# Kernel optimization log

Hardware: AMD Instinct MI355X
Metric: run time of the kernel (lower is better)

The kernel has to match this reference:

```python
import jax, jax.numpy as jnp
import numpy as np


def setup_inputs() -> dict:
    key = jax.random.key(0)
    k0, k1, k2, k3 = jax.random.split(key, 4)
    B, C = 32, 768
    t_h = t_w = 8
    s_h = s_w = 16
    N = t_h * t_w * 2 + s_h * s_w  # 384
    return {
        "x_v": jax.random.normal(k0, (B, N, C), jnp.float32),
        "x_i": jax.random.normal(k1, (B, N, C), jnp.float32),
        "qkv_w": jax.random.normal(k2, (3 * C, C), jnp.float32) * 0.02,
        "proj_w": jax.random.normal(k3, (C, C), jnp.float32) * 0.02,
        "proj_b": jnp.zeros((C,), jnp.float32),
        "t_h": t_h, "t_w": t_w, "s_h": s_h, "s_w": s_w,
        "num_heads": 12,
    }


def reference(x_v, x_i, qkv_w, proj_w, proj_b, t_h, t_w, s_h, s_w, num_heads):
    B, N, C = x_v.shape
    H = num_heads
    Dh = C // H
    scale = Dh ** (-0.5)
    mt = t_h * t_w * 2  # template tokens (two templates)

    # joint QKV projection over both modalities: [2B, N, C]
    x = jnp.concatenate([x_v, x_i], axis=0)
    qkv = (x @ qkv_w.T).reshape(2 * B, N, 3, H, Dh)
    qkv = jnp.transpose(qkv, (2, 0, 3, 1, 4))  # [3, 2B, H, N, Dh]
    q, k, v = qkv[0], qkv[1], qkv[2]
    qV, qI = q[:B], q[B:]
    kV, kI = k[:B], k[B:]
    vV, vI = v[:B], v[B:]

    q_mt_V, q_s_V = qV[:, :, :mt], qV[:, :, mt:]
    k_mt_V, k_s_V = kV[:, :, :mt], kV[:, :, mt:]
    v_mt_V, v_s_V = vV[:, :, :mt], vV[:, :, mt:]
    q_mt_I, q_s_I = qI[:, :, :mt], qI[:, :, mt:]
    k_mt_I, k_s_I = kI[:, :, :mt], kI[:, :, mt:]
    v_mt_I, v_s_I = vI[:, :, :mt], vI[:, :, mt:]

    # shared cross-modal template KV
    k_mt = jnp.concatenate([k_mt_V, k_mt_I], axis=2)
    v_mt = jnp.concatenate([v_mt_V, v_mt_I], axis=2)

    def attend(q_, k_, v_):
        a = jax.nn.softmax(jnp.einsum('bhqd,bhkd->bhqk', q_, k_) * scale, axis=-1)
        o = jnp.einsum('bhqk,bhkd->bhqd', a, v_)
        return o.transpose(0, 2, 1, 3).reshape(B, -1, C)

    # template branches: self-attention within own modality
    x_mt_V = attend(q_mt_V, k_mt_V, v_mt_V)
    x_mt_I = attend(q_mt_I, k_mt_I, v_mt_I)
    # search branches: attend to cross-modal templates + own search
    x_s_V = attend(q_s_V, jnp.concatenate([k_mt, k_s_V], axis=2),
                   jnp.concatenate([v_mt, v_s_V], axis=2))
    x_s_I = attend(q_s_I, jnp.concatenate([k_mt, k_s_I], axis=2),
                   jnp.concatenate([v_mt, v_s_I], axis=2))

    x_V = jnp.concatenate([x_mt_V, x_s_V], axis=1)
    x_I = jnp.concatenate([x_mt_I, x_s_I], axis=1)
    out = jnp.concatenate([x_V, x_I], axis=0) @ proj_w.T + proj_b
    return out[:B], out[B:]
```

## Files before the change

kernel.cpp:

```cpp
#include <hip/hip_runtime.h>

typedef __bf16 bf16;
typedef __bf16 bf16x4 __attribute__((ext_vector_type(4)));
typedef __bf16 bf16x8 __attribute__((ext_vector_type(8)));
typedef float f32x4 __attribute__((ext_vector_type(4)));

#define MFMA16(a,b,c) __builtin_amdgcn_mfma_f32_16x16x32_bf16((a),(b),(c),0,0,0)
#define SBAR() __builtin_amdgcn_s_barrier()
#define SCHED0() __builtin_amdgcn_sched_barrier(0)


__device__ inline void gload16(const bf16* g, bf16* l) {
  __builtin_amdgcn_global_load_lds(
      (const __attribute__((address_space(1))) void*)g,
      (__attribute__((address_space(3))) void*)l, 16, 0, 0);
}

__device__ inline void stage128(const bf16* __restrict__ gsrc,
                                bf16* lds_base, int tid, int wv) {
#pragma unroll
  for (int r = 0; r < 4; ++r) {
    int s = r * 256 + tid;
    int row = s >> 3;
    int chunk = (s & 7) ^ (row & 7);
    gload16(gsrc + (size_t)row * 768 + chunk * 8,
            lds_base + (size_t)(r * 256 + wv * 64) * 8);
  }
}

__device__ inline bf16x8 frag64(const bf16* buf, int row, int ks, int lg) {
  int slot = ((ks << 2) | lg) ^ (row & 7);
  return *(const bf16x8*)(buf + (size_t)row * 64 + slot * 8);
}

#define GEMM128_LOOP(APANEL, BPANEL, NTILES)                                    \
  do {                                                                          \
    stage128((APANEL), &As[0][0][0], tid, wv);                                  \
    stage128((BPANEL), &Bs[0][0][0], tid, wv);                                  \
    stage128((APANEL) + 64, &As[1][0][0], tid, wv);                             \
    stage128((BPANEL) + 64, &Bs[1][0][0], tid, wv);                             \
    asm volatile("s_waitcnt vmcnt(8)" ::: "memory"); SCHED0();                  \
    SBAR();                                                                     \
    int c = 0;                                                                  \
    for (int t = 0; t < (NTILES); ++t) {                                        \
      const bf16* Ab = &As[c][0][0];                                            \
      const bf16* Bb = &Bs[c][0][0];                                            \
      bf16x8 af[4][2], bfr[4][2];                                               \
      _Pragma("unroll")                                                         \
      for (int nf = 0; nf < 4; ++nf)                                            \
        _Pragma("unroll")                                                       \
        for (int ks = 0; ks < 2; ++ks)                                          \
          bfr[nf][ks] = frag64(Bb, wc + nf * 16 + lr, ks, lg);                  \
      _Pragma("unroll")                                                         \
      for (int mf = 0; mf < 4; ++mf)                                            \
        _Pragma("unroll")                                                       \
        for (int ks = 0; ks < 2; ++ks)                                          \
          af[mf][ks] = frag64(Ab, wr + mf * 16 + lr, ks, lg);                   \
      asm volatile("s_waitcnt lgkmcnt(0)" ::: "memory"); SCHED0();              \
      SBAR();              \
      if (t + 2 < (NTILES)) {                                                   \
        stage128((APANEL) + (t + 2) * 64, &As[c][0][0], tid, wv);               \
        stage128((BPANEL) + (t + 2) * 64, &Bs[c][0][0], tid, wv);               \
      }                                                                         \
      __builtin_amdgcn_s_setprio(1);                                            \
      _Pragma("unroll")                                                         \
      for (int mf = 0; mf < 4; ++mf)                                            \
        _Pragma("unroll")                                                       \
        for (int nf = 0; nf < 4; ++nf)                                          \
          _Pragma("unroll")                                                     \
          for (int ks = 0; ks < 2; ++ks)                                        \
            acc[mf][nf] = MFMA16(af[mf][ks], bfr[nf][ks], acc[mf][nf]);         \
      __builtin_amdgcn_s_setprio(0);                                            \
      if (t + 2 < (NTILES)) { asm volatile("s_waitcnt vmcnt(8)" ::: "memory"); }\
      else                  { asm volatile("s_waitcnt vmcnt(0)" ::: "memory"); }\
      SCHED0();                                                                 \
      SBAR();                       \
      c ^= 1;                                                                   \
    }                                                                           \
  } while (0)

__global__ __launch_bounds__(256) void convert1_kernel(
    const float* __restrict__ xv, const float* __restrict__ xi,
    const float* __restrict__ w, bf16* __restrict__ dst)
{
  const size_t NV = 9437184;
  const size_t NX = 18874368;
  const size_t NT = 20643840;
  for (size_t i = (size_t)blockIdx.x * 256 + threadIdx.x; i * 8 < NT;
       i += (size_t)gridDim.x * 256) {
    size_t e = i * 8;
    const float* src;
    if (e < NV)      src = xv + e;
    else if (e < NX) src = xi + (e - NV);
    else             src = w + (e - NX);
    f32x4 a = *(const f32x4*)src;
    f32x4 b = *(const f32x4*)(src + 4);
    bf16x8 r;
    r[0] = (bf16)a[0]; r[1] = (bf16)a[1]; r[2] = (bf16)a[2]; r[3] = (bf16)a[3];
    r[4] = (bf16)b[0]; r[5] = (bf16)b[1]; r[6] = (bf16)b[2]; r[7] = (bf16)b[3];
    *(bf16x8*)(dst + e) = r;
  }
}

__global__ __launch_bounds__(256) void convert2_kernel(
    const float* __restrict__ w, bf16* __restrict__ dst)
{
  size_t i = (size_t)blockIdx.x * 256 + threadIdx.x;
  size_t e = i * 8;
  if (e >= 589824) return;
  f32x4 a = *(const f32x4*)(w + e);
  f32x4 b = *(const f32x4*)(w + e + 4);
  bf16x8 r;
  r[0] = (bf16)a[0]; r[1] = (bf16)a[1]; r[2] = (bf16)a[2]; r[3] = (bf16)a[3];
  r[4] = (bf16)b[0]; r[5] = (bf16)b[1]; r[6] = (bf16)b[2]; r[7] = (bf16)b[3];
  *(bf16x8*)(dst + e) = r;
}

__global__ __launch_bounds__(256, 2) void qkv_kernel(
    const bf16* __restrict__ X, const bf16* __restrict__ W,
    bf16* __restrict__ Qo, bf16* __restrict__ Ko, bf16* __restrict__ VTo)
{
  __shared__ bf16 As[2][128][64];
  __shared__ bf16 Bs[2][128][64];
  int bid = blockIdx.x;
  int swz = (bid & 7) * 432 + (bid >> 3);
  const int nt = swz % 18, mt = swz / 18;
  const int m0 = mt * 128, n0 = nt * 128;
  const int tid = threadIdx.x;
  const int lane = tid & 63;
  const int wv = tid >> 6;
  const int wr = (wv >> 1) * 64, wc = (wv & 1) * 64;
  const int lr = lane & 15, lg = lane >> 4;

  const bf16* Xp = X + (size_t)m0 * 768;
  const bf16* Wp = W + (size_t)n0 * 768;

  f32x4 acc[4][4] = {};

  GEMM128_LOOP(Xp, Wp, 12);

#pragma unroll
  for (int mf = 0; mf < 4; ++mf)
#pragma unroll
    for (int nf = 0; nf < 4; ++nf) {
      int m = m0 + wr + mf * 16 + lg * 4;
      int n = n0 + wc + nf * 16 + lr;
      int bp = m / 384, tok = m - bp * 384;
      int comp = (n >= 1536) ? 2 : (n >= 768) ? 1 : 0;
      int rem = n - comp * 768;
      int hh = rem >> 6, d = rem & 63;
      if (comp == 2) {
        bf16x4 pk;
        pk[0] = (bf16)acc[mf][nf][0]; pk[1] = (bf16)acc[mf][nf][1];
        pk[2] = (bf16)acc[mf][nf][2]; pk[3] = (bf16)acc[mf][nf][3];
        *(bf16x4*)(VTo + (((size_t)bp * 12 + hh) * 64 + d) * 384 + tok) = pk;
      } else {
#pragma unroll
        for (int r = 0; r < 4; ++r) {
          size_t addr = (((size_t)bp * 12 + hh) * 384 + tok + r) * 64 + d;
          float val = acc[mf][nf][r];
          if (comp == 0) Qo[addr] = (bf16)(val * 0.125f);
          else           Ko[addr] = (bf16)val;
        }
      }
    }
}

__global__ __launch_bounds__(256) void attn_kernel(
    const bf16* __restrict__ Q, const bf16* __restrict__ K, const bf16* __restrict__ VT,
    bf16* __restrict__ ATT)
{
  __shared__ union {
    bf16 Qs[128][72];
    bf16 Ps[4][32][136];
  } u;
  __shared__ bf16 Ks[128][72];
  __shared__ bf16 VTs[64][136];

  const int bid = blockIdx.x;
  const int qb = bid % 3;
  const int h  = (bid / 3) % 12;
  const int bp = bid / 36;
  const int tid = threadIdx.x;
  const int lane = tid & 63;
  const int wv = tid >> 6;
  const int lr = lane & 15, lg = lane >> 4;

  const size_t bh384 = ((size_t)bp * 12 + h) * 384;
  const int q0 = qb * 128;

  for (int v = tid; v < 1024; v += 256) {
    int row = v >> 3, cg = (v & 7) * 8;
    *(bf16x8*)(&u.Qs[row][cg]) = *(const bf16x8*)(Q + (bh384 + q0 + row) * 64 + cg);
  }
  __syncthreads();

  bf16x8 qf[2][2];
#pragma unroll
  for (int mf = 0; mf < 2; ++mf)
#pragma unroll
    for (int ks = 0; ks < 2; ++ks)
      qf[mf][ks] = *(const bf16x8*)(&u.Qs[wv * 32 + mf * 16 + lr][ks * 32 + lg * 8]);

  f32x4 O[2][4] = {};
  float runmax[2] = {-1e30f, -1e30f}, runsum[2] = {0.f, 0.f};

  const int nchunks = (qb == 0) ? 1 : 4;
  for (int c = 0; c < nchunks; ++c) {
    int src_b, t0;
    if (qb == 0)      { src_b = bp;            t0 = 0; }
    else if (c == 0)  { src_b = bp & 31;       t0 = 0; }
    else if (c == 1)  { src_b = (bp & 31)+32;  t0 = 0; }
    else              { src_b = bp;            t0 = (c - 1) * 128; }
    const size_t kb  = (((size_t)src_b * 12 + h) * 384 + t0) * 64;
    const size_t vtb = ((size_t)src_b * 12 + h) * 64 * 384 + t0;

    __syncthreads();
    for (int v = tid; v < 1024; v += 256) {
      int row = v >> 3, cg = (v & 7) * 8;
      *(bf16x8*)(&Ks[row][cg]) = *(const bf16x8*)(K + kb + row * 64 + cg);
    }
    for (int v = tid; v < 1024; v += 256) {
      int d = v >> 4, p = (v & 15) * 8;
      *(bf16x8*)(&VTs[d][p]) = *(const bf16x8*)(VT + vtb + (size_t)d * 384 + p);
    }
    __syncthreads();

    f32x4 St[2][8] = {};
#pragma unroll
    for (int nf = 0; nf < 8; ++nf) {
#pragma unroll
      for (int ks = 0; ks < 2; ++ks) {
        bf16x8 kf = *(const bf16x8*)(&Ks[nf * 16 + lr][ks * 32 + lg * 8]);
        St[0][nf] = MFMA16(kf, qf[0][ks], St[0][nf]);
        St[1][nf] = MFMA16(kf, qf[1][ks], St[1][nf]);
      }
    }

    float rfq[2];
#pragma unroll
    for (int mf = 0; mf < 2; ++mf) {
      float mx = St[mf][0][0];
#pragma unroll
      for (int nf = 0; nf < 8; ++nf)
#pragma unroll
        for (int r = 0; r < 4; ++r) mx = fmaxf(mx, St[mf][nf][r]);
      mx = fmaxf(mx, __shfl_xor(mx, 16));
      mx = fmaxf(mx, __shfl_xor(mx, 32));
      float nm = fmaxf(runmax[mf], mx);
      rfq[mf] = __expf(runmax[mf] - nm);
      runmax[mf] = nm;
      float rs = 0.f;
#pragma unroll
      for (int nf = 0; nf < 8; ++nf)
#pragma unroll
        for (int r = 0; r < 4; ++r) {
          float p = __expf(St[mf][nf][r] - nm);
          St[mf][nf][r] = p;
          rs += p;
        }
      rs += __shfl_xor(rs, 16);
      rs += __shfl_xor(rs, 32);
      runsum[mf] = runsum[mf] * rfq[mf] + rs;
    }

#pragma unroll
    for (int mf = 0; mf < 2; ++mf)
#pragma unroll
      for (int nf = 0; nf < 8; ++nf) {
        bf16x4 pk;
        pk[0] = (bf16)St[mf][nf][0]; pk[1] = (bf16)St[mf][nf][1];
        pk[2] = (bf16)St[mf][nf][2]; pk[3] = (bf16)St[mf][nf][3];
        *(bf16x4*)(&u.Ps[wv][mf * 16 + lr][nf * 16 + lg * 4]) = pk;
      }

#pragma unroll
    for (int mf = 0; mf < 2; ++mf)
#pragma unroll
      for (int r = 0; r < 4; ++r) {
        float rr = __shfl(rfq[mf], (lg * 4 + r) + (lg << 4));
#pragma unroll
        for (int vn = 0; vn < 4; ++vn) O[mf][vn][r] *= rr;
      }

#pragma unroll
    for (int ks = 0; ks < 4; ++ks) {
      bf16x8 pf0 = *(const bf16x8*)(&u.Ps[wv][lr][ks * 32 + lg * 8]);
      bf16x8 pf1 = *(const bf16x8*)(&u.Ps[wv][16 + lr][ks * 32 + lg * 8]);
#pragma unroll
      for (int vn = 0; vn < 4; ++vn) {
        bf16x8 vf = *(const bf16x8*)(&VTs[vn * 16 + lr][ks * 32 + lg * 8]);
        O[0][vn] = MFMA16(pf0, vf, O[0][vn]);
        O[1][vn] = MFMA16(pf1, vf, O[1][vn]);
      }
    }
  }

#pragma unroll
  for (int mf = 0; mf < 2; ++mf) {
#pragma unroll
    for (int r = 0; r < 4; ++r) {
      float rs = __shfl(runsum[mf], (lg * 4 + r) + (lg << 4));
      float inv = 1.0f / rs;
#pragma unroll
      for (int vn = 0; vn < 4; ++vn) {
        int tok = q0 + wv * 32 + mf * 16 + lg * 4 + r;
        int d = vn * 16 + lr;
        ATT[((size_t)bp * 384 + tok) * 768 + h * 64 + d] = (bf16)(O[mf][vn][r] * inv);
      }
    }
  }
}

__global__ __launch_bounds__(256, 2) void proj_kernel(
    const bf16* __restrict__ A, const bf16* __restrict__ W,
    const float* __restrict__ bias, float* __restrict__ out)
{
  __shared__ bf16 As[2][128][64];
  __shared__ bf16 Bs[2][128][64];
  int bid = blockIdx.x;
  int swz = (bid & 7) * 144 + (bid >> 3);
  const int nt = swz % 6, mt = swz / 6;
  const int m0 = mt * 128, n0 = nt * 128;
  const int tid = threadIdx.x;
  const int lane = tid & 63;
  const int wv = tid >> 6;
  const int wr = (wv >> 1) * 64, wc = (wv & 1) * 64;
  const int lr = lane & 15, lg = lane >> 4;

  const bf16* Ap = A + (size_t)m0 * 768;
  const bf16* Wpp = W + (size_t)n0 * 768;

  f32x4 acc[4][4] = {};

  GEMM128_LOOP(Ap, Wpp, 12);

#pragma unroll
  for (int mf = 0; mf < 4; ++mf)
#pragma unroll
    for (int nf = 0; nf < 4; ++nf)
#pragma unroll
      for (int r = 0; r < 4; ++r) {
        int m = m0 + wr + mf * 16 + lg * 4 + r;
        int n = n0 + wc + nf * 16 + lr;
        out[(size_t)m * 768 + n] = acc[mf][nf][r] + bias[n];
      }
}

extern "C" void kernel_launch(void* const* d_in, const int* in_sizes, int n_in,
                              void* d_out, int out_size, void* d_ws, size_t ws_size,
                              hipStream_t stream) {
  (void)in_sizes; (void)n_in; (void)out_size; (void)ws_size;
  const float* xv     = (const float*)d_in[0];
  const float* xi     = (const float*)d_in[1];
  const float* qkv_w  = (const float*)d_in[2];
  const float* proj_w = (const float*)d_in[3];
  const float* proj_b = (const float*)d_in[4];
  float* out = (float*)d_out;

  bf16* Xb = (bf16*)d_out;
  bf16* Wq = Xb + (size_t)18874368;

  const size_t SZ = (size_t)64 * 12 * 384 * 64;
  bf16* Q   = (bf16*)d_ws;
  bf16* K   = Q + SZ;
  bf16* VT  = K + SZ;
  bf16* ATT = VT + SZ;
  bf16* Wp  = Q;

  convert1_kernel<<<2048, 256, 0, stream>>>(xv, xi, qkv_w, Xb);
  qkv_kernel<<<3456, 256, 0, stream>>>(Xb, Wq, Q, K, VT);
  attn_kernel<<<64 * 12 * 3, 256, 0, stream>>>(Q, K, VT, ATT);
  convert2_kernel<<<288, 256, 0, stream>>>(proj_w, Wp);
  proj_kernel<<<1152, 256, 0, stream>>>(ATT, Wp, proj_b, out);
}
```

Before: 270.3 us.

## Prefetch next K/V chunk into registers in attention; use nontemporal stores

The attention kernel now loads the next chunk's K and V^T tiles into registers while the current chunk's QK^T and softmax/PV math runs, then writes them to LDS at the top of the next iteration. This hides global load latency behind compute at the cost of 8 extra bf16x8 registers per thread. Separately, the convert, QKV, and projection kernels switch their global writes to nontemporal stores. The aim is to avoid polluting caches with data consumed later, but the Q/K/V outputs are reread soon by attention, so bypassing the cache could also hurt.

```diff
diff --git a/kernel.cpp b/kernel.cpp
--- a/kernel.cpp
+++ b/kernel.cpp
@@ -98,7 +98,7 @@
     bf16x8 r;
     r[0] = (bf16)a[0]; r[1] = (bf16)a[1]; r[2] = (bf16)a[2]; r[3] = (bf16)a[3];
     r[4] = (bf16)b[0]; r[5] = (bf16)b[1]; r[6] = (bf16)b[2]; r[7] = (bf16)b[3];
-    *(bf16x8*)(dst + e) = r;
+    __builtin_nontemporal_store(r, (bf16x8*)(dst + e));
   }
 }
 
@@ -113,7 +113,7 @@
   bf16x8 r;
   r[0] = (bf16)a[0]; r[1] = (bf16)a[1]; r[2] = (bf16)a[2]; r[3] = (bf16)a[3];
   r[4] = (bf16)b[0]; r[5] = (bf16)b[1]; r[6] = (bf16)b[2]; r[7] = (bf16)b[3];
-  *(bf16x8*)(dst + e) = r;
+  __builtin_nontemporal_store(r, (bf16x8*)(dst + e));
 }
 
 __global__ __launch_bounds__(256, 2) void qkv_kernel(
@@ -153,14 +153,17 @@
         bf16x4 pk;
         pk[0] = (bf16)acc[mf][nf][0]; pk[1] = (bf16)acc[mf][nf][1];
         pk[2] = (bf16)acc[mf][nf][2]; pk[3] = (bf16)acc[mf][nf][3];
-        *(bf16x4*)(VTo + (((size_t)bp * 12 + hh) * 64 + d) * 384 + tok) = pk;
+        __builtin_nontemporal_store(
+            pk, (bf16x4*)(VTo + (((size_t)bp * 12 + hh) * 64 + d) * 384 + tok));
       } else {
 #pragma unroll
         for (int r = 0; r < 4; ++r) {
           size_t addr = (((size_t)bp * 12 + hh) * 384 + tok + r) * 64 + d;
           float val = acc[mf][nf][r];
-          if (comp == 0) Qo[addr] = (bf16)(val * 0.125f);
-          else           Ko[addr] = (bf16)val;
+          if (comp == 0)
+            __builtin_nontemporal_store((bf16)(val * 0.125f), Qo + addr);
+          else
+            __builtin_nontemporal_store((bf16)val, Ko + addr);
         }
       }
     }
@@ -188,6 +191,17 @@
 
   const size_t bh384 = ((size_t)bp * 12 + h) * 384;
   const int q0 = qb * 128;
+  const int nchunks = (qb == 0) ? 1 : 4;
+
+  auto chunk_base = [&](int c, size_t& kb, size_t& vtb) {
+    int src_b, t0;
+    if (qb == 0)      { src_b = bp;             t0 = 0; }
+    else if (c == 0)  { src_b = bp & 31;        t0 = 0; }
+    else if (c == 1)  { src_b = (bp & 31) + 32; t0 = 0; }
+    else              { src_b = bp;             t0 = (c - 1) * 128; }
+    kb  = (((size_t)src_b * 12 + h) * 384 + t0) * 64;
+    vtb = ((size_t)src_b * 12 + h) * 64 * 384 + t0;
+  };
 
   for (int v = tid; v < 1024; v += 256) {
     int row = v >> 3, cg = (v & 7) * 8;
@@ -202,29 +216,38 @@
     for (int ks = 0; ks < 2; ++ks)
       qf[mf][ks] = *(const bf16x8*)(&u.Qs[wv * 32 + mf * 16 + lr][ks * 32 + lg * 8]);
 
+  const int krow = tid >> 3,  kcg = (tid & 7) * 8;
+  const int vd   = tid >> 4,  vp  = (tid & 15) * 8;
+  bf16x8 kreg[4], vreg[4];
+  {
+    size_t kb, vtb; chunk_base(0, kb, vtb);
+#pragma unroll
+    for (int i = 0; i < 4; ++i) {
+      kreg[i] = *(const bf16x8*)(K + kb + (size_t)(krow + i * 32) * 64 + kcg);
+      vreg[i] = *(const bf16x8*)(VT + vtb + (size_t)(vd + i * 16) * 384 + vp);
+    }
+  }
+
   f32x4 O[2][4] = {};
   float runmax[2] = {-1e30f, -1e30f}, runsum[2] = {0.f, 0.f};
 
-  const int nchunks = (qb == 0) ? 1 : 4;
   for (int c = 0; c < nchunks; ++c) {
-    int src_b, t0;
-    if (qb == 0)      { src_b = bp;            t0 = 0; }
-    else if (c == 0)  { src_b = bp & 31;       t0 = 0; }
-    else if (c == 1)  { src_b = (bp & 31)+32;  t0 = 0; }
-    else              { src_b = bp;            t0 = (c - 1) * 128; }
-    const size_t kb  = (((size_t)src_b * 12 + h) * 384 + t0) * 64;
-    const size_t vtb = ((size_t)src_b * 12 + h) * 64 * 384 + t0;
-
     __syncthreads();
-    for (int v = tid; v < 1024; v += 256) {
-      int row = v >> 3, cg = (v & 7) * 8;
-      *(bf16x8*)(&Ks[row][cg]) = *(const bf16x8*)(K + kb + row * 64 + cg);
-    }
-    for (int v = tid; v < 1024; v += 256) {
-      int d = v >> 4, p = (v & 15) * 8;
-      *(bf16x8*)(&VTs[d][p]) = *(const bf16x8*)(VT + vtb + (size_t)d * 384 + p);
+#pragma unroll
+    for (int i = 0; i < 4; ++i) {
+      *(bf16x8*)(&Ks[krow + i * 32][kcg]) = kreg[i];
+      *(bf16x8*)(&VTs[vd + i * 16][vp])   = vreg[i];
     }
     __syncthreads();
+
+    if (c + 1 < nchunks) {
+      size_t kb, vtb; chunk_base(c + 1, kb, vtb);
+#pragma unroll
+      for (int i = 0; i < 4; ++i) {
+        kreg[i] = *(const bf16x8*)(K + kb + (size_t)(krow + i * 32) * 64 + kcg);
+        vreg[i] = *(const bf16x8*)(VT + vtb + (size_t)(vd + i * 16) * 384 + vp);
+      }
+    }
 
     f32x4 St[2][8] = {};
 #pragma unroll
@@ -343,7 +366,8 @@
       for (int r = 0; r < 4; ++r) {
         int m = m0 + wr + mf * 16 + lg * 4 + r;
         int n = n0 + wc + nf * 16 + lr;
-        out[(size_t)m * 768 + n] = acc[mf][nf][r] + bias[n];
+        __builtin_nontemporal_store(acc[mf][nf][r] + bias[n],
+                                    out + (size_t)m * 768 + n);
       }
 }
 
```

Result: slower. 288.9 us (+6.9%).
